# Kernel tuning notes

Hardware: AMD Instinct MI355X
Metric: run time of the kernel (lower is better)

## Reference

```python
import jax, jax.numpy as jnp
import numpy as np

B, T, F = 4096, 64, 32
U1, U2 = 256, 128  # stacked GRU: rnn_units, rnn_units // 2


def _gru_layer(x, Wg, bg, Wc, bc, units):
    """TF GRUCell semantics over a full sequence.
    x: [B, T, D]. Wg: [D+U, 2U], Wc: [D+U, U]. Returns outputs [B, T, U].
    r,u = sigmoid([x,h] Wg + bg); c = tanh([x, r*h] Wc + bc); h' = u*h + (1-u)*c
    """
    xT = jnp.swapaxes(x, 0, 1)  # [T, B, D]
    h0 = jnp.zeros((x.shape[0], units), x.dtype)

    def step(h, xt):
        gates = jax.nn.sigmoid(jnp.concatenate([xt, h], axis=-1) @ Wg + bg)
        r, u = jnp.split(gates, 2, axis=-1)
        c = jnp.tanh(jnp.concatenate([xt, r * h], axis=-1) @ Wc + bc)
        h_new = u * h + (1.0 - u) * c
        return h_new, h_new

    _, outs = jax.lax.scan(step, h0, xT)
    return jnp.swapaxes(outs, 0, 1)  # [B, T, U]


def setup_inputs() -> dict:
    key = jax.random.key(0)
    ks = jax.random.split(key, 12)
    s = 0.1
    inp = {
        "frames": jax.random.normal(ks[0], (B, T, F), jnp.float32),
        "W1_g": jax.random.normal(ks[1], (F + U1, 2 * U1), jnp.float32) * s,
        "b1_g": jnp.ones((2 * U1,), jnp.float32),  # TF gate bias init = 1.0
        "W1_c": jax.random.normal(ks[2], (F + U1, U1), jnp.float32) * s,
        "b1_c": jnp.zeros((U1,), jnp.float32),
        "W2_g": jax.random.normal(ks[3], (U1 + U2, 2 * U2), jnp.float32) * s,
        "b2_g": jnp.ones((2 * U2,), jnp.float32),
        "W2_c": jax.random.normal(ks[4], (U1 + U2, U2), jnp.float32) * s,
        "b2_c": jnp.zeros((U2,), jnp.float32),
        "Wd": jax.random.normal(ks[5], (U2, F), jnp.float32) * s,
        "bd": jnp.zeros((F,), jnp.float32),
    }
    return inp


def reference(frames, W1_g, b1_g, W1_c, b1_c, W2_g, b2_g, W2_c, b2_c, Wd, bd):
    # stacked GRU: MultiRNNCell([GRUCell(U1), GRUCell(U1 // 2)])
    h1 = _gru_layer(frames, W1_g, b1_g, W1_c, b1_c, U1)   # [B, T, U1]
    h2 = _gru_layer(h1, W2_g, b2_g, W2_c, b2_c, U2)       # [B, T, U2]
    last = h2[:, -1]                                       # use_cell_state=False -> outputs[:, -1]
    predicted = last @ Wd + bd                             # dense to sensor_count
    return predicted
```

## Files before the change

### kernel.cpp

```cpp
#include <hip/hip_runtime.h>


typedef unsigned short u16;
typedef unsigned int u32;
typedef __attribute__((ext_vector_type(8))) short bhalf8;
typedef __attribute__((ext_vector_type(4))) float fx4;

constexpr int Bc = 4096, Tc = 64, Fc = 32, U1 = 256, U2 = 128;
constexpr int K1 = Fc + U1;
constexpr int K2 = U1 + U2;
constexpr int NB = 16, NTHR = 512;
constexpr int LD1 = 296;
constexpr int LD2 = 392;
constexpr int LDR1 = 264;
constexpr int LDR2 = 136;

constexpr int nW1g = K1 * 512, nW1c = K1 * 256, nW2g = K2 * 256, nW2c = K2 * 128;
constexpr int oW1g = 0;
constexpr int oW1c = oW1g + nW1g;
constexpr int oW2g = oW1c + nW1c;
constexpr int oW2c = oW2g + nW2g;
constexpr int WTOT = oW2c + nW2c;
constexpr int nWdT = Fc * U2;

constexpr int oA1h = 0;
constexpr int oA1l = oA1h + 16 * LD1;
constexpr int oA2h = oA1l + 16 * LD1;
constexpr int oA2l = oA2h + 16 * LD2;
constexpr int oR1h = oA2l + 16 * LD2;
constexpr int oR1l = oR1h + 16 * LDR1;
constexpr int oR2h = oR1l + 16 * LDR1;
constexpr int oR2l = oR2h + 16 * LDR2;
constexpr int SM_TOT = oR2l + 16 * LDR2;
constexpr size_t SMEM_BYTES = (size_t)SM_TOT * 2;

#define LGKM_BARRIER() asm volatile("s_waitcnt lgkmcnt(0)\n\ts_barrier" ::: "memory")

__device__ __forceinline__ u16 bf16_rne(float x) {
  unsigned u = __float_as_uint(x);
  return (u16)((u + 0x7fffu + ((u >> 16) & 1u)) >> 16);
}
__device__ __forceinline__ float bf16_f(u16 h) {
  return __uint_as_float(((unsigned)h) << 16);
}
__device__ __forceinline__ float sigm(float x) { return 1.0f / (1.0f + __expf(-x)); }
__device__ __forceinline__ float tanh_(float x) {
  x = fminf(fmaxf(x, -15.0f), 15.0f);
  const float s = __expf(2.0f * x);
  return (s - 1.0f) / (s + 1.0f);
}

__global__ void prep_weights(const float* __restrict__ W1g, const float* __restrict__ W1c,
                             const float* __restrict__ W2g, const float* __restrict__ W2c,
                             const float* __restrict__ Wd, u16* __restrict__ ws) {
  int j = blockIdx.x * 256 + threadIdx.x;
  if (j >= WTOT + nWdT) return;
  if (j >= WTOT) {
    const int jj = j - WTOT;
    float* wdT = (float*)(ws + WTOT);
    const int o = jj >> 7, c = jj & 127;
    wdT[jj] = Wd[c * Fc + o];
    return;
  }
  const float* src; u16* dst; int K, N, jj;
  if (j < nW1g)                    { src = W1g; K = K1; N = 512; jj = j;                      dst = ws + oW1g; }
  else if (j < nW1g + nW1c)        { src = W1c; K = K1; N = 256; jj = j - nW1g;               dst = ws + oW1c; }
  else if (j < nW1g + nW1c + nW2g) { src = W2g; K = K2; N = 256; jj = j - nW1g - nW1c;        dst = ws + oW2g; }
  else                             { src = W2c; K = K2; N = 128; jj = j - nW1g - nW1c - nW2g; dst = ws + oW2c; }
  int n = jj / K, k = jj - n * K;
  dst[(size_t)n * K + k] = bf16_rne(src[(size_t)k * N + n]);
}

template <int NT, int D, int KT>
struct Pipe {
  const u16* wp[NT];
  bhalf8 bb[D][NT];
  __device__ __forceinline__ void init(const u16* __restrict__ W, const int* n0,
                                       int K, int lc, int ao) {
#pragma unroll
    for (int i = 0; i < NT; ++i) wp[i] = W + (size_t)(n0[i] + lc) * K + ao;
  }
  __device__ __forceinline__ void prefetch() {
#pragma unroll
    for (int d = 0; d < D; ++d)
#pragma unroll
      for (int i = 0; i < NT; ++i) bb[d][i] = *(const bhalf8*)(wp[i] + d * 32);
  }
  __device__ __forceinline__ void roll(int kt) {
    if (kt + D < KT) {
#pragma unroll
      for (int i = 0; i < NT; ++i) bb[kt % D][i] = *(const bhalf8*)(wp[i] + (kt + D) * 32);
    }
  }
};

template <int NT, int D, int KT, typename P, typename LD>
__device__ __forceinline__ void run_mm(P& p, fx4 (&acc)[NT], LD&& ld) {
#pragma unroll
  for (int kt = 0; kt < KT; ++kt) {
    bhalf8 ah, al;
    ld(kt, ah, al);
#pragma unroll
    for (int i = 0; i < NT; ++i) {
      acc[i] = __builtin_amdgcn_mfma_f32_16x16x32_bf16(ah, p.bb[kt % D][i], acc[i], 0, 0, 0);
      acc[i] = __builtin_amdgcn_mfma_f32_16x16x32_bf16(al, p.bb[kt % D][i], acc[i], 0, 0, 0);
    }
    p.roll(kt);
  }
}

__global__ __launch_bounds__(NTHR, 2)
void gru_mfma(const float* __restrict__ frames, const u16* __restrict__ ws,
              const float* __restrict__ b1g, const float* __restrict__ b1c,
              const float* __restrict__ b2g, const float* __restrict__ b2c,
              const float* __restrict__ bd, float* __restrict__ out) {
  extern __shared__ u16 sm[];

  const int tid = threadIdx.x;
  const int w = tid >> 6;
  const int l = tid & 63;
  const int lc = l & 15;
  const int lk = l >> 4;
  const int ao = lk * 8;
  const int row0 = lk * 4;
  const int b0 = blockIdx.x * NB;

  const float bg1r0 = b1g[w * 32 + lc],       bg1r1 = b1g[w * 32 + 16 + lc];
  const float bg1u0 = b1g[256 + w * 32 + lc], bg1u1 = b1g[256 + w * 32 + 16 + lc];
  const float bc10  = b1c[w * 32 + lc],       bc11  = b1c[w * 32 + 16 + lc];
  const float bg2r  = b2g[w * 16 + lc],       bg2u  = b2g[128 + w * 16 + lc];
  const float bc2v  = b2c[w * 16 + lc];

  Pipe<4, 4, 9> pG1;  Pipe<2, 6, 9> pC1;  Pipe<2, 6, 12> pG2;  Pipe<1, 8, 12> pC2;
  const int n0g1[4] = {w * 32, w * 32 + 16, 256 + w * 32, 256 + w * 32 + 16};
  const int n0c1[2] = {w * 32, w * 32 + 16};
  const int n0g2[2] = {w * 16, 128 + w * 16};
  const int n0c2[1] = {w * 16};
  pG1.init(ws + oW1g, n0g1, K1, lc, ao);
  pC1.init(ws + oW1c, n0c1, K1, lc, ao);
  pG2.init(ws + oW2g, n0g2, K2, lc, ao);
  pC2.init(ws + oW2c, n0c2, K2, lc, ao);

  for (int i = tid; i < SM_TOT; i += NTHR) sm[i] = 0;

  const int xb = tid >> 5, xf = tid & 31;
  const float* fptr = frames + (size_t)(b0 + xb) * (Tc * Fc) + xf;

  {
    const float x0 = fptr[0];
    const u16 h = bf16_rne(x0);
    sm[oA1h + xb * LD1 + xf] = h;
    sm[oA1l + xb * LD1 + xf] = bf16_rne(x0 - bf16_f(h));
  }
  pG1.prefetch();
  LGKM_BARRIER();

  auto ldG1 = [&](int kt, bhalf8& ah, bhalf8& al) {
    const int idx = lc * LD1 + kt * 32 + ao;
    ah = *(const bhalf8*)&sm[oA1h + idx];
    al = *(const bhalf8*)&sm[oA1l + idx];
  };
  auto ldC1 = [&](int kt, bhalf8& ah, bhalf8& al) {
    if (kt == 0) {
      const int idx = lc * LD1 + ao;
      ah = *(const bhalf8*)&sm[oA1h + idx];
      al = *(const bhalf8*)&sm[oA1l + idx];
    } else {
      const int idx = lc * LDR1 + (kt - 1) * 32 + ao;
      ah = *(const bhalf8*)&sm[oR1h + idx];
      al = *(const bhalf8*)&sm[oR1l + idx];
    }
  };
  auto ldG2 = [&](int kt, bhalf8& ah, bhalf8& al) {
    const int idx = lc * LD2 + kt * 32 + ao;
    ah = *(const bhalf8*)&sm[oA2h + idx];
    al = *(const bhalf8*)&sm[oA2l + idx];
  };
  auto ldC2 = [&](int kt, bhalf8& ah, bhalf8& al) {
    if (kt < 8) {
      const int idx = lc * LD2 + kt * 32 + ao;
      ah = *(const bhalf8*)&sm[oA2h + idx];
      al = *(const bhalf8*)&sm[oA2l + idx];
    } else {
      const int idx = lc * LDR2 + (kt - 8) * 32 + ao;
      ah = *(const bhalf8*)&sm[oR2h + idx];
      al = *(const bhalf8*)&sm[oR2l + idx];
    }
  };

  for (int t = 0; t < Tc; ++t) {
    const float xn = (t + 1 < Tc) ? fptr[(t + 1) * Fc] : 0.0f;

    fx4 acc[4] = { {bg1r0, bg1r0, bg1r0, bg1r0}, {bg1r1, bg1r1, bg1r1, bg1r1},
                   {bg1u0, bg1u0, bg1u0, bg1u0}, {bg1u1, bg1u1, bg1u1, bg1u1} };
    run_mm<4, 4, 9>(pG1, acc, ldG1);
    pC1.prefetch();

    float hold1[2][4], uu[2][4];
#pragma unroll
    for (int i = 0; i < 2; ++i)
#pragma unroll
      for (int q = 0; q < 4; ++q) {
        const int row = row0 + q, col = w * 32 + i * 16 + lc;
        hold1[i][q] = bf16_f(sm[oA1h + row * LD1 + Fc + col]) +
                      bf16_f(sm[oA1l + row * LD1 + Fc + col]);
        uu[i][q] = sigm(acc[2 + i][q]);
      }
#pragma unroll
    for (int i = 0; i < 2; ++i)
#pragma unroll
      for (int q = 0; q < 4; ++q) {
        const int row = row0 + q, col = w * 32 + i * 16 + lc;
        const float rh = sigm(acc[i][q]) * hold1[i][q];
        const u16 hh = bf16_rne(rh);
        sm[oR1h + row * LDR1 + col] = hh;
        sm[oR1l + row * LDR1 + col] = bf16_rne(rh - bf16_f(hh));
      }
    LGKM_BARRIER();

    fx4 accc[2] = { {bc10, bc10, bc10, bc10}, {bc11, bc11, bc11, bc11} };
    run_mm<2, 6, 9>(pC1, accc, ldC1);
    pG2.prefetch();

#pragma unroll
    for (int i = 0; i < 2; ++i)
#pragma unroll
      for (int q = 0; q < 4; ++q) {
        const int row = row0 + q, col = w * 32 + i * 16 + lc;
        const float c = tanh_(accc[i][q]);
        const float hn = c + uu[i][q] * (hold1[i][q] - c);
        const u16 hh = bf16_rne(hn);
        const u16 hl = bf16_rne(hn - bf16_f(hh));
        sm[oA1h + row * LD1 + Fc + col] = hh;
        sm[oA1l + row * LD1 + Fc + col] = hl;
        sm[oA2h + row * LD2 + col] = hh;
        sm[oA2l + row * LD2 + col] = hl;
      }
    LGKM_BARRIER();

    fx4 acc2[2] = { {bg2r, bg2r, bg2r, bg2r}, {bg2u, bg2u, bg2u, bg2u} };
    run_mm<2, 6, 12>(pG2, acc2, ldG2);
    pC2.prefetch();

    float hold2[4], uu2[4];
#pragma unroll
    for (int q = 0; q < 4; ++q) {
      const int row = row0 + q, col = w * 16 + lc;
      hold2[q] = bf16_f(sm[oA2h + row * LD2 + U1 + col]) +
                 bf16_f(sm[oA2l + row * LD2 + U1 + col]);
      uu2[q] = sigm(acc2[1][q]);
    }
#pragma unroll
    for (int q = 0; q < 4; ++q) {
      const int row = row0 + q, col = w * 16 + lc;
      const float rh = sigm(acc2[0][q]) * hold2[q];
      const u16 hh = bf16_rne(rh);
      sm[oR2h + row * LDR2 + col] = hh;
      sm[oR2l + row * LDR2 + col] = bf16_rne(rh - bf16_f(hh));
    }
    {
      const u16 h = bf16_rne(xn);
      sm[oA1h + xb * LD1 + xf] = h;
      sm[oA1l + xb * LD1 + xf] = bf16_rne(xn - bf16_f(h));
    }
    LGKM_BARRIER();

    fx4 acc3[1] = { {bc2v, bc2v, bc2v, bc2v} };
    run_mm<1, 8, 12>(pC2, acc3, ldC2);
    pG1.prefetch();

#pragma unroll
    for (int q = 0; q < 4; ++q) {
      const int row = row0 + q, col = w * 16 + lc;
      const float c = tanh_(acc3[0][q]);
      const float hn = c + uu2[q] * (hold2[q] - c);
      const u16 hh = bf16_rne(hn);
      sm[oA2h + row * LD2 + U1 + col] = hh;
      sm[oA2l + row * LD2 + U1 + col] = bf16_rne(hn - bf16_f(hh));
    }
    LGKM_BARRIER();
  }

  {
    const float* wdT = (const float*)(ws + WTOT);
    const int o = tid & 31, b = tid >> 5;
    const float4* wrow = (const float4*)(wdT + o * 128);
    float acc = bd[o];
#pragma unroll 8
    for (int c4 = 0; c4 < 32; ++c4) {
      const float4 wv = wrow[c4];
      const int c = c4 * 4;
      const int base = b * LD2 + U1 + c;
      const float h0 = bf16_f(sm[oA2h + base + 0]) + bf16_f(sm[oA2l + base + 0]);
      const float h1 = bf16_f(sm[oA2h + base + 1]) + bf16_f(sm[oA2l + base + 1]);
      const float h2 = bf16_f(sm[oA2h + base + 2]) + bf16_f(sm[oA2l + base + 2]);
      const float h3 = bf16_f(sm[oA2h + base + 3]) + bf16_f(sm[oA2l + base + 3]);
      acc = fmaf(h0, wv.x, fmaf(h1, wv.y, fmaf(h2, wv.z, fmaf(h3, wv.w, acc))));
    }
    out[(size_t)(b0 + b) * Fc + o] = acc;
  }
}

extern "C" void kernel_launch(void* const* d_in, const int* in_sizes, int n_in,
                              void* d_out, int out_size, void* d_ws, size_t ws_size,
                              hipStream_t stream) {
  const float* frames = (const float*)d_in[0];
  const float* W1g = (const float*)d_in[1];
  const float* b1g = (const float*)d_in[2];
  const float* W1c = (const float*)d_in[3];
  const float* b1c = (const float*)d_in[4];
  const float* W2g = (const float*)d_in[5];
  const float* b2g = (const float*)d_in[6];
  const float* W2c = (const float*)d_in[7];
  const float* b2c = (const float*)d_in[8];
  const float* Wd  = (const float*)d_in[9];
  const float* bd  = (const float*)d_in[10];
  u16* ws = (u16*)d_ws;
  float* outp = (float*)d_out;

  hipFuncSetAttribute(reinterpret_cast<const void*>(gru_mfma),
                      hipFuncAttributeMaxDynamicSharedMemorySize, (int)SMEM_BYTES);

  hipLaunchKernelGGL(prep_weights, dim3((WTOT + nWdT + 255) / 256), dim3(256), 0, stream,
                     W1g, W1c, W2g, W2c, Wd, ws);
  hipLaunchKernelGGL(gru_mfma, dim3(Bc / NB), dim3(NTHR), SMEM_BYTES, stream,
                     frames, ws, b1g, b1c, b2g, b2c, bd, outp);
}
```

Baseline: 947.5 us.

## Double workgroup to 16 waves and split GRU gate columns across waves

Raises the block size from 512 to 1024 threads so each wave owns 16 gate columns instead of 32, halving the per-wave MFMA tiles for layer 1. In layer 2, waves 0-7 compute the update gate and candidate while waves 8-15 compute the reset gate and write r*h. The goal is shorter per-step critical-path latency in the serial recurrence and more latency hiding. In exchange it adds register pressure under launch bounds of 4, halves the per-thread register budget, and leaves half the waves idle during the final candidate matmul.

```diff
diff --git a/kernel.cpp b/kernel.cpp
--- a/kernel.cpp
+++ b/kernel.cpp
@@ -2,14 +2,13 @@
 
 
 typedef unsigned short u16;
-typedef unsigned int u32;
 typedef __attribute__((ext_vector_type(8))) short bhalf8;
 typedef __attribute__((ext_vector_type(4))) float fx4;
 
 constexpr int Bc = 4096, Tc = 64, Fc = 32, U1 = 256, U2 = 128;
 constexpr int K1 = Fc + U1;
 constexpr int K2 = U1 + U2;
-constexpr int NB = 16, NTHR = 512;
+constexpr int NB = 16, NTHR = 1024;
 constexpr int LD1 = 296;
 constexpr int LD2 = 392;
 constexpr int LDR1 = 264;
@@ -109,7 +108,7 @@
   }
 }
 
-__global__ __launch_bounds__(NTHR, 2)
+__global__ __launch_bounds__(NTHR, 4)
 void gru_mfma(const float* __restrict__ frames, const u16* __restrict__ ws,
               const float* __restrict__ b1g, const float* __restrict__ b1c,
               const float* __restrict__ b2g, const float* __restrict__ b2c,
@@ -124,18 +123,19 @@
   const int ao = lk * 8;
   const int row0 = lk * 4;
   const int b0 = blockIdx.x * NB;
-
-  const float bg1r0 = b1g[w * 32 + lc],       bg1r1 = b1g[w * 32 + 16 + lc];
-  const float bg1u0 = b1g[256 + w * 32 + lc], bg1u1 = b1g[256 + w * 32 + 16 + lc];
-  const float bc10  = b1c[w * 32 + lc],       bc11  = b1c[w * 32 + 16 + lc];
-  const float bg2r  = b2g[w * 16 + lc],       bg2u  = b2g[128 + w * 16 + lc];
-  const float bc2v  = b2c[w * 16 + lc];
-
-  Pipe<4, 4, 9> pG1;  Pipe<2, 6, 9> pC1;  Pipe<2, 6, 12> pG2;  Pipe<1, 8, 12> pC2;
-  const int n0g1[4] = {w * 32, w * 32 + 16, 256 + w * 32, 256 + w * 32 + 16};
-  const int n0c1[2] = {w * 32, w * 32 + 16};
-  const int n0g2[2] = {w * 16, 128 + w * 16};
-  const int n0c2[1] = {w * 16};
+  const int w2 = w & 7;
+
+  const float bR  = b1g[w * 16 + lc];
+  const float bU  = b1g[256 + w * 16 + lc];
+  const float bC1 = b1c[w * 16 + lc];
+  const float bG2 = (w < 8) ? b2g[128 + w2 * 16 + lc] : b2g[w2 * 16 + lc];
+  const float bC2 = b2c[w2 * 16 + lc];
+
+  Pipe<2, 4, 9> pG1;  Pipe<1, 6, 9> pC1;  Pipe<1, 6, 12> pG2;  Pipe<1, 8, 12> pC2;
+  const int n0g1[2] = {w * 16, 256 + w * 16};
+  const int n0c1[1] = {w * 16};
+  const int n0g2[1] = {(w < 8) ? (128 + w2 * 16) : (w2 * 16)};
+  const int n0c2[1] = {w2 * 16};
   pG1.init(ws + oW1g, n0g1, K1, lc, ao);
   pC1.init(ws + oW1c, n0c1, K1, lc, ao);
   pG2.init(ws + oW2g, n0g2, K2, lc, ao);
@@ -143,10 +143,11 @@
 
   for (int i = tid; i < SM_TOT; i += NTHR) sm[i] = 0;
 
-  const int xb = tid >> 5, xf = tid & 31;
+  const bool stager = tid < 512;
+  const int xb = (tid >> 5) & 15, xf = tid & 31;
   const float* fptr = frames + (size_t)(b0 + xb) * (Tc * Fc) + xf;
 
-  {
+  if (stager) {
     const float x0 = fptr[0];
     const u16 h = bf16_rne(x0);
     sm[oA1h + xb * LD1 + xf] = h;
@@ -189,99 +190,97 @@
   };
 
   for (int t = 0; t < Tc; ++t) {
-    const float xn = (t + 1 < Tc) ? fptr[(t + 1) * Fc] : 0.0f;
-
-    fx4 acc[4] = { {bg1r0, bg1r0, bg1r0, bg1r0}, {bg1r1, bg1r1, bg1r1, bg1r1},
-                   {bg1u0, bg1u0, bg1u0, bg1u0}, {bg1u1, bg1u1, bg1u1, bg1u1} };
-    run_mm<4, 4, 9>(pG1, acc, ldG1);
+    const float xn = (stager && t + 1 < Tc) ? fptr[(t + 1) * Fc] : 0.0f;
+
+    fx4 acc[2] = { {bR, bR, bR, bR}, {bU, bU, bU, bU} };
+    run_mm<2, 4, 9>(pG1, acc, ldG1);
     pC1.prefetch();
 
-    float hold1[2][4], uu[2][4];
-#pragma unroll
-    for (int i = 0; i < 2; ++i)
-#pragma unroll
-      for (int q = 0; q < 4; ++q) {
-        const int row = row0 + q, col = w * 32 + i * 16 + lc;
-        hold1[i][q] = bf16_f(sm[oA1h + row * LD1 + Fc + col]) +
-                      bf16_f(sm[oA1l + row * LD1 + Fc + col]);
-        uu[i][q] = sigm(acc[2 + i][q]);
-      }
-#pragma unroll
-    for (int i = 0; i < 2; ++i)
-#pragma unroll
-      for (int q = 0; q < 4; ++q) {
-        const int row = row0 + q, col = w * 32 + i * 16 + lc;
-        const float rh = sigm(acc[i][q]) * hold1[i][q];
-        const u16 hh = bf16_rne(rh);
-        sm[oR1h + row * LDR1 + col] = hh;
-        sm[oR1l + row * LDR1 + col] = bf16_rne(rh - bf16_f(hh));
-      }
-    LGKM_BARRIER();
-
-    fx4 accc[2] = { {bc10, bc10, bc10, bc10}, {bc11, bc11, bc11, bc11} };
-    run_mm<2, 6, 9>(pC1, accc, ldC1);
-    pG2.prefetch();
-
-#pragma unroll
-    for (int i = 0; i < 2; ++i)
-#pragma unroll
-      for (int q = 0; q < 4; ++q) {
-        const int row = row0 + q, col = w * 32 + i * 16 + lc;
-        const float c = tanh_(accc[i][q]);
-        const float hn = c + uu[i][q] * (hold1[i][q] - c);
-        const u16 hh = bf16_rne(hn);
-        const u16 hl = bf16_rne(hn - bf16_f(hh));
-        sm[oA1h + row * LD1 + Fc + col] = hh;
-        sm[oA1l + row * LD1 + Fc + col] = hl;
-        sm[oA2h + row * LD2 + col] = hh;
-        sm[oA2l + row * LD2 + col] = hl;
-      }
-    LGKM_BARRIER();
-
-    fx4 acc2[2] = { {bg2r, bg2r, bg2r, bg2r}, {bg2u, bg2u, bg2u, bg2u} };
-    run_mm<2, 6, 12>(pG2, acc2, ldG2);
-    pC2.prefetch();
-
-    float hold2[4], uu2[4];
+    float hold1[4], uu[4];
 #pragma unroll
     for (int q = 0; q < 4; ++q) {
       const int row = row0 + q, col = w * 16 + lc;
+      hold1[q] = bf16_f(sm[oA1h + row * LD1 + Fc + col]) +
+                 bf16_f(sm[oA1l + row * LD1 + Fc + col]);
+      uu[q] = sigm(acc[1][q]);
+    }
+#pragma unroll
+    for (int q = 0; q < 4; ++q) {
+      const int row = row0 + q, col = w * 16 + lc;
+      const float rh = sigm(acc[0][q]) * hold1[q];
+      const u16 hh = bf16_rne(rh);
+      sm[oR1h + row * LDR1 + col] = hh;
+      sm[oR1l + row * LDR1 + col] = bf16_rne(rh - bf16_f(hh));
+    }
+    LGKM_BARRIER();
+
+    fx4 accc[1] = { {bC1, bC1, bC1, bC1} };
+    run_mm<1, 6, 9>(pC1, accc, ldC1);
+    pG2.prefetch();
+
+#pragma unroll
+    for (int q = 0; q < 4; ++q) {
+      const int row = row0 + q, col = w * 16 + lc;
+      const float c = tanh_(accc[0][q]);
+      const float hn = c + uu[q] * (hold1[q] - c);
+      const u16 hh = bf16_rne(hn);
+      const u16 hl = bf16_rne(hn - bf16_f(hh));
+      sm[oA1h + row * LD1 + Fc + col] = hh;
+      sm[oA1l + row * LD1 + Fc + col] = hl;
+      sm[oA2h + row * LD2 + col] = hh;
+      sm[oA2l + row * LD2 + col] = hl;
+    }
+    LGKM_BARRIER();
+
+    fx4 acc2[1] = { {bG2, bG2, bG2, bG2} };
+    run_mm<1, 6, 12>(pG2, acc2, ldG2);
+    if (w < 8) pC2.prefetch();
+
+    float hold2[4], uu2[4];
+#pragma unroll
+    for (int q = 0; q < 4; ++q) {
+      const int row = row0 + q, col = w2 * 16 + lc;
       hold2[q] = bf16_f(sm[oA2h + row * LD2 + U1 + col]) +
                  bf16_f(sm[oA2l + row * LD2 + U1 + col]);
-      uu2[q] = sigm(acc2[1][q]);
-    }
-#pragma unroll
-    for (int q = 0; q < 4; ++q) {
-      const int row = row0 + q, col = w * 16 + lc;
-      const float rh = sigm(acc2[0][q]) * hold2[q];
-      const u16 hh = bf16_rne(rh);
-      sm[oR2h + row * LDR2 + col] = hh;
-      sm[oR2l + row * LDR2 + col] = bf16_rne(rh - bf16_f(hh));
-    }
-    {
+      uu2[q] = sigm(acc2[0][q]);
+    }
+    if (w >= 8) {
+#pragma unroll
+      for (int q = 0; q < 4; ++q) {
+        const int row = row0 + q, col = w2 * 16 + lc;
+        const float rh = uu2[q] * hold2[q];
+        const u16 hh = bf16_rne(rh);
+        sm[oR2h + row * LDR2 + col] = hh;
+        sm[oR2l + row * LDR2 + col] = bf16_rne(rh - bf16_f(hh));
+      }
+    }
+    if (stager) {
       const u16 h = bf16_rne(xn);
       sm[oA1h + xb * LD1 + xf] = h;
       sm[oA1l + xb * LD1 + xf] = bf16_rne(xn - bf16_f(h));
     }
     LGKM_BARRIER();
 
-    fx4 acc3[1] = { {bc2v, bc2v, bc2v, bc2v} };
-    run_mm<1, 8, 12>(pC2, acc3, ldC2);
+    fx4 acc3[1] = { {bC2, bC2, bC2, bC2} };
+    if (w < 8) {
+      run_mm<1, 8, 12>(pC2, acc3, ldC2);
+    }
     pG1.prefetch();
-
-#pragma unroll
-    for (int q = 0; q < 4; ++q) {
-      const int row = row0 + q, col = w * 16 + lc;
-      const float c = tanh_(acc3[0][q]);
-      const float hn = c + uu2[q] * (hold2[q] - c);
-      const u16 hh = bf16_rne(hn);
-      sm[oA2h + row * LD2 + U1 + col] = hh;
-      sm[oA2l + row * LD2 + U1 + col] = bf16_rne(hn - bf16_f(hh));
+    if (w < 8) {
+#pragma unroll
+      for (int q = 0; q < 4; ++q) {
+        const int row = row0 + q, col = w2 * 16 + lc;
+        const float c = tanh_(acc3[0][q]);
+        const float hn = c + uu2[q] * (hold2[q] - c);
+        const u16 hh = bf16_rne(hn);
+        sm[oA2h + row * LD2 + U1 + col] = hh;
+        sm[oA2l + row * LD2 + U1 + col] = bf16_rne(hn - bf16_f(hh));
+      }
     }
     LGKM_BARRIER();
   }
 
-  {
+  if (tid < 512) {
     const float* wdT = (const float*)(ws + WTOT);
     const int o = tid & 31, b = tid >> 5;
     const float4* wrow = (const float4*)(wdT + o * 128);
```

Result: slower. 1.388 ms (+46.4%).
